# Kernel optimization log

Hardware: AMD Instinct MI355X
Metric: run time of the kernel (lower is better)

## Reference

```python
import jax, jax.numpy as jnp
import numpy as np
from jax import lax

B, C, H, W = 8, 19, 512, 512
LOW_T, HIGH_T = 100.0, 200.0  # cv2.Canny(img, 100, 200)
MAX_HYST_ITERS = 256          # safety cap on hysteresis fixed-point iterations

_KX = jnp.array([[-1., 0., 1.], [-2., 0., 2.], [-1., 0., 1.]], jnp.float32)
_KY = jnp.array([[-1., -2., -1.], [0., 0., 0.], [1., 2., 1.]], jnp.float32)


def _conv3(x, k):
    # x: [B, H+2, W+2] (already padded), k: [3,3] -> [B, H, W]
    return lax.conv_general_dilated(x[:, None], k[None, None], (1, 1), 'VALID')[:, 0]


def _dilate3(s):
    # 8-connected boolean dilation via 3x3 max window
    return lax.reduce_window(s.astype(jnp.int32), 0, lax.max, (1, 3, 3), (1, 1, 1), 'SAME') > 0


def _canny(img):
    # img: [B, H, W] float values in [0, 255]. Returns float32 edge map in {0,1}.
    b, h, w = img.shape
    pad = jnp.pad(img, ((0, 0), (1, 1), (1, 1)), mode='edge')
    gx = _conv3(pad, _KX)
    gy = _conv3(pad, _KY)
    mag = jnp.abs(gx) + jnp.abs(gy)  # cv2 default L1 gradient magnitude
    ang = jnp.degrees(jnp.arctan2(gy, gx)) % 180.0
    mp = jnp.pad(mag, ((0, 0), (1, 1), (1, 1)))
    nb = lambda dy, dx: mp[:, 1 + dy:1 + dy + h, 1 + dx:1 + dx + w]
    # non-maximum suppression along quantized gradient direction
    d0 = (ang < 22.5) | (ang >= 157.5)
    d45 = (ang >= 22.5) & (ang < 67.5)
    d90 = (ang >= 67.5) & (ang < 112.5)
    keep0 = (mag >= nb(0, 1)) & (mag >= nb(0, -1))
    keep45 = (mag >= nb(-1, 1)) & (mag >= nb(1, -1))
    keep90 = (mag >= nb(1, 0)) & (mag >= nb(-1, 0))
    keep135 = (mag >= nb(-1, -1)) & (mag >= nb(1, 1))
    keep = jnp.where(d0, keep0, jnp.where(d45, keep45, jnp.where(d90, keep90, keep135)))
    strong = keep & (mag > HIGH_T)
    weak = keep & (mag > LOW_T)  # weak includes strong
    # hysteresis: propagate strong labels through weak pixels to fixed point
    def cond(c):
        s, changed, it = c
        return changed & (it < MAX_HYST_ITERS)
    def body(c):
        s, _, it = c
        s2 = (weak & _dilate3(s)) | strong
        return (s2, jnp.any(s2 != s), it + 1)
    edges, _, _ = lax.while_loop(cond, body, (strong, jnp.array(True), jnp.array(0)))
    return edges.astype(jnp.float32)


def setup_inputs() -> dict:
    key = jax.random.key(0)
    k1, k2 = jax.random.split(key)
    pred = jax.random.normal(k1, (B, C, H, W), dtype=jnp.float32)
    labels = jax.random.uniform(k2, (B, H, W), dtype=jnp.float32)
    return {'pred': pred, 'labels': labels}


def reference(pred, labels):
    # pred_convert: per-pixel argmax over channel dim -> class ids [B, H, W]
    cls = jnp.argmax(pred, axis=1)
    # canny(): (img * 255).astype('uint8') -- class ids wrap mod 256
    img_p = ((cls * 255) % 256).astype(jnp.float32)
    # labels in [0,1): uint8 cast truncates toward zero
    img_l = jnp.floor(labels * 255.0)
    ep = _canny(img_p)  # [B, H, W] in {0,1}
    el = _canny(img_l)  # [B, H, W] in {0,1}
    # nn.CrossEntropyLoss() on float target of same shape: input [N=B, C=H, d1=W],
    # target is class probabilities; mean over N and d1.
    logp = jax.nn.log_softmax(ep, axis=1)
    return jnp.mean(jnp.sum(-el * logp, axis=1))
```

## Files before the change

### kernel.cpp

```cpp
#include <hip/hip_runtime.h>
#include <hip/hip_bf16.h>
#include <math.h>

typedef unsigned long long u64;
typedef unsigned char u8;
typedef unsigned short u16;
typedef unsigned int u32;

#define BB 8
#define CC 19
#define HH 512
#define WW 512
#define HWSZ (HH*WW)
#define NIMG 16

__global__ __launch_bounds__(256) void k_pre(const float* __restrict__ pred,
                                             const float* __restrict__ lab,
                                             u8* __restrict__ img,
                                             float* __restrict__ out) {
    int idx = blockIdx.x * 256 + threadIdx.x;
    if (idx == 0) out[0] = 0.0f;
    int p4 = idx * 4;
    int b = p4 / HWSZ;
    int rem = p4 - b * HWSZ;
    const float4* base = (const float4*)(pred + (size_t)b * CC * HWSZ + rem);
    float4 best = base[0];
    int ix = 0, iy = 0, iz = 0, iw = 0;
    for (int c = 1; c < CC; ++c) {
        float4 v = base[(size_t)c * (HWSZ / 4)];
        if (v.x > best.x) { best.x = v.x; ix = c; }
        if (v.y > best.y) { best.y = v.y; iy = c; }
        if (v.z > best.z) { best.z = v.z; iz = c; }
        if (v.w > best.w) { best.w = v.w; iw = c; }
    }
    uchar4 o;
    o.x = (u8)(-ix); o.y = (u8)(-iy); o.z = (u8)(-iz); o.w = (u8)(-iw);
    *(uchar4*)(img + p4) = o;
    float4 v = *(const float4*)(lab + p4);
    uchar4 ol;
    ol.x = (u8)(v.x * 255.0f);
    ol.y = (u8)(v.y * 255.0f);
    ol.z = (u8)(v.z * 255.0f);
    ol.w = (u8)(v.w * 255.0f);
    *(uchar4*)(img + (size_t)BB * HWSZ + p4) = ol;
}

__device__ __forceinline__ void sobel8(const u8* __restrict__ base, int yy, int x0,
                                       int mag8[8], u32* dirpack) {
    int r0 = (yy == 0) ? 0 : yy - 1;
    int r2 = (yy == 511) ? 511 : yy + 1;
    const u8* rps[3] = { base + r0 * WW, base + yy * WW, base + r2 * WW };
    int bb[3][10];
#pragma unroll
    for (int r = 0; r < 3; ++r) {
        u64 m = *(const u64*)(rps[r] + x0);
        bb[r][0] = (x0 == 0) ? rps[r][0] : rps[r][x0 - 1];
#pragma unroll
        for (int i = 0; i < 8; ++i) bb[r][i + 1] = (int)((m >> (8 * i)) & 0xFF);
        bb[r][9] = (x0 == 504) ? rps[r][511] : rps[r][x0 + 8];
    }
    u32 dp = 0;
#pragma unroll
    for (int i = 0; i < 8; ++i) {
        int a00 = bb[0][i], a01 = bb[0][i + 1], a02 = bb[0][i + 2];
        int a10 = bb[1][i],                     a12 = bb[1][i + 2];
        int a20 = bb[2][i], a21 = bb[2][i + 1], a22 = bb[2][i + 2];
        int gx = (a02 + 2 * a12 + a22) - (a00 + 2 * a10 + a20);
        int gy = (a20 + 2 * a21 + a22) - (a00 + 2 * a01 + a02);
        int ax = gx < 0 ? -gx : gx;
        int ay = gy < 0 ? -gy : gy;
        mag8[i] = ax + ay;
        if (dirpack) {
            float fax = (float)ax, fay = (float)ay;
            u32 dir;
            if (fay < 0.41421356237309515f * fax) dir = 0;
            else if (fay >= 2.414213562373095f * fax) dir = 2;
            else dir = ((gx ^ gy) >= 0) ? 1u : 3u;
            dp |= dir << (2 * i);
        }
    }
    if (dirpack) *dirpack = dp;
}

__global__ __launch_bounds__(256) void k_gradnms(const u8* __restrict__ imgs,
                                                 u64* __restrict__ weak,
                                                 u64* __restrict__ strong) {
    __shared__ u16 smag[6][514];
    __shared__ alignas(8) u8 wb[4][64];
    __shared__ alignas(8) u8 sb[4][64];
    int im = blockIdx.x >> 7;
    int y0 = (blockIdx.x & 127) * 4;
    int r    = threadIdx.x >> 6;
    int lane = threadIdx.x & 63;
    int x0 = lane * 8;
    const u8* base = imgs + (size_t)im * HWSZ;

    if (threadIdx.x < 6) { smag[threadIdx.x][0] = 0; smag[threadIdx.x][513] = 0; }

    int y = y0 + r;
    int mag8[8]; u32 dp;
    sobel8(base, y, x0, mag8, &dp);
#pragma unroll
    for (int i = 0; i < 8; ++i) smag[r + 1][1 + x0 + i] = (u16)mag8[i];

    if (r == 0) {
        if (y0 > 0) {
            int m2[8]; sobel8(base, y0 - 1, x0, m2, nullptr);
#pragma unroll
            for (int i = 0; i < 8; ++i) smag[0][1 + x0 + i] = (u16)m2[i];
        } else {
#pragma unroll
            for (int i = 0; i < 8; ++i) smag[0][1 + x0 + i] = 0;
        }
    } else if (r == 3) {
        if (y0 + 4 < 512) {
            int m2[8]; sobel8(base, y0 + 4, x0, m2, nullptr);
#pragma unroll
            for (int i = 0; i < 8; ++i) smag[5][1 + x0 + i] = (u16)m2[i];
        } else {
#pragma unroll
            for (int i = 0; i < 8; ++i) smag[5][1 + x0 + i] = 0;
        }
    }
    __syncthreads();

    int wbits = 0, sbits = 0;
#pragma unroll
    for (int i = 0; i < 8; ++i) {
        int x = x0 + i;
        int mag = mag8[i];
        int dir = (int)((dp >> (2 * i)) & 3u);
        int n1, n2;
        switch (dir) {
            case 0:  n1 = smag[r + 1][x];     n2 = smag[r + 1][x + 2]; break;
            case 1:  n1 = smag[r][x + 2];     n2 = smag[r + 2][x];     break;
            case 2:  n1 = smag[r][x + 1];     n2 = smag[r + 2][x + 1]; break;
            default: n1 = smag[r][x];         n2 = smag[r + 2][x + 2]; break;
        }
        int keep = (mag >= n1) & (mag >= n2);
        wbits |= (keep & (mag > 100)) << i;
        sbits |= (keep & (mag > 200)) << i;
    }
    wb[r][lane] = (u8)wbits;
    sb[r][lane] = (u8)sbits;
    __syncthreads();

    if (threadIdx.x < 32) {
        int rr = threadIdx.x >> 3;
        int w  = threadIdx.x & 7;
        u64 W = *(const u64*)&wb[rr][w * 8];
        u64 S = *(const u64*)&sb[rr][w * 8];
        size_t o = ((size_t)im * HH + (y0 + rr)) * 8 + w;
        weak[o] = W;
        strong[o] = S;
    }
}

__global__ __launch_bounds__(512) void k_hyst(const u64* __restrict__ weakg,
                                              const u64* __restrict__ strongg,
                                              u64* __restrict__ edges) {
    __shared__ u32 hlo[8][512];
    __shared__ u32 hhi[8][512];
    __shared__ int flags[2];
    int y = threadIdx.x;
    int im = blockIdx.x;
    size_t base = ((size_t)im * HH + y) * 8;
    u64 wk[8], s[8];
#pragma unroll
    for (int j = 0; j < 8; ++j) {
        wk[j] = weakg[base + j];
        s[j] = strongg[base + j];
    }
    for (int it = 0; it < 256; ++it) {
        u64 diff = 0;
        u64 c = 0;
#pragma unroll
        for (int j = 0; j < 8; ++j) {
            u64 a = s[j], w = wk[j];
            u64 t1 = a + w;       u64 c1 = (u64)(t1 < a);
            u64 t2 = t1 + c;      u64 c2 = (u64)(t2 < t1);
            u64 ns = a | ((t2 ^ w) & w);
            diff |= ns ^ a;
            s[j] = ns;
            c = c1 | c2;
        }
        c = 0;
#pragma unroll
        for (int j = 7; j >= 0; --j) {
            u64 a = __builtin_bitreverse64(s[j]);
            u64 w = __builtin_bitreverse64(wk[j]);
            u64 t1 = a + w;       u64 c1 = (u64)(t1 < a);
            u64 t2 = t1 + c;      u64 c2 = (u64)(t2 < t1);
            u64 nsr = a | ((t2 ^ w) & w);
            u64 ns = __builtin_bitreverse64(nsr);
            diff |= ns ^ s[j];
            s[j] = ns;
            c = c1 | c2;
        }
        u64 hh[8];
#pragma unroll
        for (int j = 0; j < 8; ++j) hh[j] = s[j] | (s[j] << 1) | (s[j] >> 1);
#pragma unroll
        for (int j = 1; j < 8; ++j) hh[j] |= s[j - 1] >> 63;
#pragma unroll
        for (int j = 0; j < 7; ++j) hh[j] |= s[j + 1] << 63;
#pragma unroll
        for (int j = 0; j < 8; ++j) {
            hlo[j][y] = (u32)hh[j];
            hhi[j][y] = (u32)(hh[j] >> 32);
        }
        if (y == 0 && it == 0) flags[0] = 0;
        __syncthreads();
        if (y == 0) flags[(it + 1) & 1] = 0;
#pragma unroll
        for (int j = 0; j < 8; ++j) {
            u64 up = (y > 0)   ? ((u64)hlo[j][y - 1] | ((u64)hhi[j][y - 1] << 32)) : 0ull;
            u64 dn = (y < 511) ? ((u64)hlo[j][y + 1] | ((u64)hhi[j][y + 1] << 32)) : 0ull;
            u64 t = wk[j] & (up | dn) & ~s[j];
            diff |= t;
            s[j] |= t;
        }
        if (diff) flags[it & 1] = 1;
        __syncthreads();
        if (!flags[it & 1]) break;
    }
#pragma unroll
    for (int j = 0; j < 8; ++j) edges[base + j] = s[j];
}

__global__ __launch_bounds__(256) void k_loss(const u64* __restrict__ edges,
                                              float* __restrict__ out) {
    int b = blockIdx.x >> 3;
    int j = blockIdx.x & 7;
    int wave = threadIdx.x >> 6;
    int lane = threadIdx.x & 63;
    const u64* ep = edges + ((size_t)b * HH) * 8 + j;
    const u64* el = edges + ((size_t)(b + 8) * HH) * 8 + j;
    int k = 0, es = 0, ov = 0;
    int y0 = wave * 128;
    for (int y = y0; y < y0 + 128; ++y) {
        u64 wp = ep[(size_t)y * 8];
        u64 wl = el[(size_t)y * 8];
        int bp = (int)((wp >> lane) & 1ull);
        int bl = (int)((wl >> lane) & 1ull);
        k += bp; es += bl; ov += (bp & bl);
    }
    __shared__ int red[3][4][64];
    red[0][wave][lane] = k;
    red[1][wave][lane] = es;
    red[2][wave][lane] = ov;
    __syncthreads();
    if (threadIdx.x < 64) {
        int l = threadIdx.x;
        int K = red[0][0][l] + red[0][1][l] + red[0][2][l] + red[0][3][l];
        int E = red[1][0][l] + red[1][1][l] + red[1][2][l] + red[1][3][l];
        int O = red[2][0][l] + red[2][1][l] + red[2][2][l] + red[2][3][l];
        float logZ = logf(512.0f + 1.7182818284590452f * (float)K);
        float v = ((float)E * logZ - (float)O) * (1.0f / 4096.0f);
#pragma unroll
        for (int o = 32; o > 0; o >>= 1) v += __shfl_down(v, o, 64);
        if (l == 0) atomicAdd(out, v);
    }
}

extern "C" void kernel_launch(void* const* d_in, const int* in_sizes, int n_in,
                              void* d_out, int out_size, void* d_ws, size_t ws_size,
                              hipStream_t stream) {
    const float* pred = (const float*)d_in[0];
    const float* labels = (const float*)d_in[1];
    float* out = (float*)d_out;

    u8*  imgs   = (u8*)d_ws;
    u64* weak   = (u64*)((char*)d_ws + (size_t)NIMG * HWSZ);
    u64* strong = (u64*)((char*)weak + (size_t)NIMG * HH * 8 * 8);
    u64* edges  = (u64*)((char*)strong + (size_t)NIMG * HH * 8 * 8);

    hipLaunchKernelGGL(k_pre, dim3(BB * HWSZ / 4 / 256), dim3(256), 0, stream,
                       pred, labels, imgs, out);
    hipLaunchKernelGGL(k_gradnms, dim3(NIMG * 128), dim3(256), 0, stream,
                       imgs, weak, strong);
    hipLaunchKernelGGL(k_hyst, dim3(NIMG), dim3(512), 0, stream,
                       weak, strong, edges);
    hipLaunchKernelGGL(k_loss, dim3(64), dim3(256), 0, stream, edges, out);
}
```

Measured before the change: 249.3 us.

## Fuse loss reduction into hysteresis kernel via inter-block flags; nontemporal pred loads

Removes the separate loss kernel. Each hysteresis block publishes a global completion flag, and blocks for prediction images wait on the matching label image's flag before computing the per-column cross-entropy terms and atomically adding them to the output. Flags are zeroed in the preprocessing kernel. The argmax loads of pred also become nontemporal vector loads to avoid polluting cache with streaming data. This saves one kernel launch and its dependency gap. In exchange it relies on all 16 blocks being co-resident for the spin-wait, and the loss now runs on only 8 blocks with 512 threads each.

```diff
diff --git a/kernel.cpp b/kernel.cpp
--- a/kernel.cpp
+++ b/kernel.cpp
@@ -6,6 +6,7 @@
 typedef unsigned char u8;
 typedef unsigned short u16;
 typedef unsigned int u32;
+typedef float fvec4 __attribute__((ext_vector_type(4)));
 
 #define BB 8
 #define CC 19
@@ -17,17 +18,19 @@
 __global__ __launch_bounds__(256) void k_pre(const float* __restrict__ pred,
                                              const float* __restrict__ lab,
                                              u8* __restrict__ img,
+                                             u32* __restrict__ flags,
                                              float* __restrict__ out) {
     int idx = blockIdx.x * 256 + threadIdx.x;
     if (idx == 0) out[0] = 0.0f;
+    if (idx < NIMG) flags[idx] = 0u;
     int p4 = idx * 4;
     int b = p4 / HWSZ;
     int rem = p4 - b * HWSZ;
-    const float4* base = (const float4*)(pred + (size_t)b * CC * HWSZ + rem);
-    float4 best = base[0];
+    const fvec4* base = (const fvec4*)(pred + (size_t)b * CC * HWSZ + rem);
+    fvec4 best = __builtin_nontemporal_load(&base[0]);
     int ix = 0, iy = 0, iz = 0, iw = 0;
     for (int c = 1; c < CC; ++c) {
-        float4 v = base[(size_t)c * (HWSZ / 4)];
+        fvec4 v = __builtin_nontemporal_load(&base[(size_t)c * (HWSZ / 4)]);
         if (v.x > best.x) { best.x = v.x; ix = c; }
         if (v.y > best.y) { best.y = v.y; iy = c; }
         if (v.z > best.z) { best.z = v.z; iz = c; }
@@ -158,10 +161,12 @@
 
 __global__ __launch_bounds__(512) void k_hyst(const u64* __restrict__ weakg,
                                               const u64* __restrict__ strongg,
-                                              u64* __restrict__ edges) {
+                                              u64* __restrict__ edges,
+                                              u32* __restrict__ flags,
+                                              float* __restrict__ out) {
     __shared__ u32 hlo[8][512];
     __shared__ u32 hhi[8][512];
-    __shared__ int flags[2];
+    __shared__ int bflags[2];
     int y = threadIdx.x;
     int im = blockIdx.x;
     size_t base = ((size_t)im * HH + y) * 8;
@@ -209,9 +214,9 @@
             hlo[j][y] = (u32)hh[j];
             hhi[j][y] = (u32)(hh[j] >> 32);
         }
-        if (y == 0 && it == 0) flags[0] = 0;
+        if (y == 0 && it == 0) bflags[0] = 0;
         __syncthreads();
-        if (y == 0) flags[(it + 1) & 1] = 0;
+        if (y == 0) bflags[(it + 1) & 1] = 0;
 #pragma unroll
         for (int j = 0; j < 8; ++j) {
             u64 up = (y > 0)   ? ((u64)hlo[j][y - 1] | ((u64)hhi[j][y - 1] << 32)) : 0ull;
@@ -220,41 +225,34 @@
             diff |= t;
             s[j] |= t;
         }
-        if (diff) flags[it & 1] = 1;
+        if (diff) bflags[it & 1] = 1;
         __syncthreads();
-        if (!flags[it & 1]) break;
+        if (!bflags[it & 1]) break;
     }
 #pragma unroll
     for (int j = 0; j < 8; ++j) edges[base + j] = s[j];
-}
-
-__global__ __launch_bounds__(256) void k_loss(const u64* __restrict__ edges,
-                                              float* __restrict__ out) {
-    int b = blockIdx.x >> 3;
-    int j = blockIdx.x & 7;
-    int wave = threadIdx.x >> 6;
-    int lane = threadIdx.x & 63;
-    const u64* ep = edges + ((size_t)b * HH) * 8 + j;
-    const u64* el = edges + ((size_t)(b + 8) * HH) * 8 + j;
-    int k = 0, es = 0, ov = 0;
-    int y0 = wave * 128;
-    for (int y = y0; y < y0 + 128; ++y) {
-        u64 wp = ep[(size_t)y * 8];
-        u64 wl = el[(size_t)y * 8];
-        int bp = (int)((wp >> lane) & 1ull);
-        int bl = (int)((wl >> lane) & 1ull);
-        k += bp; es += bl; ov += (bp & bl);
-    }
-    __shared__ int red[3][4][64];
-    red[0][wave][lane] = k;
-    red[1][wave][lane] = es;
-    red[2][wave][lane] = ov;
+    __threadfence();
     __syncthreads();
-    if (threadIdx.x < 64) {
-        int l = threadIdx.x;
-        int K = red[0][0][l] + red[0][1][l] + red[0][2][l] + red[0][3][l];
-        int E = red[1][0][l] + red[1][1][l] + red[1][2][l] + red[1][3][l];
-        int O = red[2][0][l] + red[2][1][l] + red[2][2][l] + red[2][3][l];
+    if (threadIdx.x == 0) atomicExch(&flags[im], 1u);
+
+    if (im < 8) {
+        if (threadIdx.x == 0) {
+            while (atomicAdd(&flags[im + 8], 0u) == 0u) { __builtin_amdgcn_s_sleep(8); }
+        }
+        __syncthreads();
+        __threadfence();
+        int g = threadIdx.x >> 6;
+        int l = threadIdx.x & 63;
+        const u64* ep = edges + (size_t)im * HH * 8 + g;
+        const u64* el = edges + (size_t)(im + 8) * HH * 8 + g;
+        int K = 0, E = 0, O = 0;
+        for (int yy = 0; yy < 512; ++yy) {
+            u64 wp = ep[(size_t)yy * 8];
+            u64 wl = el[(size_t)yy * 8];
+            int bp = (int)((wp >> l) & 1ull);
+            int bl = (int)((wl >> l) & 1ull);
+            K += bp; E += bl; O += (bp & bl);
+        }
         float logZ = logf(512.0f + 1.7182818284590452f * (float)K);
         float v = ((float)E * logZ - (float)O) * (1.0f / 4096.0f);
 #pragma unroll
@@ -274,12 +272,12 @@
     u64* weak   = (u64*)((char*)d_ws + (size_t)NIMG * HWSZ);
     u64* strong = (u64*)((char*)weak + (size_t)NIMG * HH * 8 * 8);
     u64* edges  = (u64*)((char*)strong + (size_t)NIMG * HH * 8 * 8);
+    u32* flags  = (u32*)((char*)edges + (size_t)NIMG * HH * 8 * 8);
 
     hipLaunchKernelGGL(k_pre, dim3(BB * HWSZ / 4 / 256), dim3(256), 0, stream,
-                       pred, labels, imgs, out);
+                       pred, labels, imgs, flags, out);
     hipLaunchKernelGGL(k_gradnms, dim3(NIMG * 128), dim3(256), 0, stream,
                        imgs, weak, strong);
     hipLaunchKernelGGL(k_hyst, dim3(NIMG), dim3(512), 0, stream,
-                       weak, strong, edges);
-    hipLaunchKernelGGL(k_loss, dim3(64), dim3(256), 0, stream, edges, out);
-}
+                       weak, strong, edges, flags, out);
+}
```

Measured after the change: 292.8 us. 1.17x slower.
